# Performance work log

Hardware: AMD Instinct MI355X
Metric: run time of the kernel (lower is better)

The kernel has to match this reference:

```python
import jax, jax.numpy as jnp
import numpy as np

B, S, D_IN, D_OUT = 4, 8192, 1024, 1024


def setup_inputs() -> dict:
    key = jax.random.key(0)
    k1, k2, k3, k4 = jax.random.split(key, 4)
    x = jax.random.normal(k1, (B, S, D_IN), dtype=jnp.float32)
    # signed int8 weights, stored int8 as in the torch buffer
    weight_int = jax.random.randint(k2, (D_OUT, D_IN), -128, 128, dtype=jnp.int32).astype(jnp.int8)
    # realistic per-output-channel scales
    weight_scale = jax.random.uniform(k3, (D_OUT,), dtype=jnp.float32, minval=0.005, maxval=0.02)
    input_scale = jnp.asarray(0.05, dtype=jnp.float32)
    bias = jax.random.normal(k4, (D_OUT,), dtype=jnp.float32) * 0.01
    return {"x": x, "weight_int": weight_int, "weight_scale": weight_scale,
            "input_scale": input_scale, "bias": bias}


def reference(x, weight_int, weight_scale, input_scale, bias):
    # quantize activations to int8 (faithful: round, clamp, cast)
    x_int = jnp.clip(jnp.round(x / input_scale), -128, 127).astype(jnp.int8)
    # module upcasts both operands to fp32 for the matmul
    out = jnp.matmul(x_int.astype(jnp.float32), weight_int.astype(jnp.float32).T)
    # dequantize: per-output-channel weight scale * scalar input scale, then bias
    out = out * weight_scale * input_scale + bias
    return out
```

## Files before the change

### kernel.cpp

```cpp
#include <hip/hip_runtime.h>
#include <stdint.h>
#include <stddef.h>

typedef int   v4i __attribute__((ext_vector_type(4)));
typedef float v4f __attribute__((ext_vector_type(4)));

#define BM 128
#define BN 128
#define BKB 128
#define M_DIM 32768
#define N_DIM 1024
#define K_DIM 1024

typedef const __attribute__((address_space(1))) void gvoid_t;
typedef __attribute__((address_space(3))) void lvoid_t;

__device__ __forceinline__ void gload16(const void* g, void* l) {
    __builtin_amdgcn_global_load_lds((gvoid_t*)g, (lvoid_t*)l, 16, 0, 0);
}

__global__ __launch_bounds__(256)
void repack_w_kernel(const int* __restrict__ wi, int* __restrict__ wq, int n4)
{
    int i = blockIdx.x * blockDim.x + threadIdx.x;
    if (i < n4) {
        v4i v = ((const v4i*)wi)[i];
        wq[i] = (v[0] & 255) | ((v[1] & 255) << 8) |
                ((v[2] & 255) << 16) | ((v[3] & 255) << 24);
    }
}

__global__ __launch_bounds__(256, 2)
void quant_kernel(const float* __restrict__ x, int* __restrict__ q,
                  const float* __restrict__ iscale_p, int n4)
{
    const float is = *iscale_p;
    int idx = blockIdx.x * blockDim.x + threadIdx.x;
    int stride = gridDim.x * blockDim.x;
    const v4f* xp = (const v4f*)x;
    for (int i = idx; i < n4; i += stride) {
        v4f v = xp[i];
        int r = 0;
        #pragma unroll
        for (int j = 0; j < 4; ++j) {
            float t = rintf(v[j] / is);
            t = fminf(127.f, fmaxf(-128.f, t));
            r |= ((int)t & 255) << (8 * j);
        }
        q[i] = r;
    }
}

__global__ __launch_bounds__(256, 2)
void qgemm_kernel(const signed char* __restrict__ Aq,
                  const signed char* __restrict__ W,
                  const float* __restrict__ wscale,
                  const float* __restrict__ iscale_p,
                  const float* __restrict__ bias,
                  float* __restrict__ out)
{
    __shared__ signed char lA[BM * BKB];
    __shared__ signed char lB[BN * BKB];

    const int nwg = gridDim.x;
    const int bid = blockIdx.x;
    const int wg  = (bid & 7) * (nwg >> 3) + (bid >> 3);
    const int m_blk = wg >> 3;
    const int n_blk = wg & 7;
    const int mrow0 = m_blk * BM;
    const int ncol0 = n_blk * BN;

    const int tid = threadIdx.x;
    const int wv  = tid >> 6;
    const int ln  = tid & 63;
    const int wm  = wv >> 1;
    const int wn  = wv & 1;
    const int lrow = ln & 15;
    const int lk16 = (ln >> 4) << 4;
    const int swz  = (lrow & 7) << 4;

    v4i acc[4][4] = {};

    for (int kt = 0; kt < K_DIM; kt += BKB) {
        __syncthreads();
        #pragma unroll
        for (int c = 0; c < 4; ++c) {
            const int o   = c * 4096 + wv * 1024 + ln * 16;
            const int row = o >> 7;
            const int inr = (o & 127) ^ ((row & 7) << 4);
            gload16(Aq + (size_t)(mrow0 + row) * K_DIM + kt + inr,
                    (void*)(lA + c * 4096 + wv * 1024));
            gload16(W + (size_t)(ncol0 + row) * K_DIM + kt + inr,
                    (void*)(lB + c * 4096 + wv * 1024));
        }
        __syncthreads();
        #pragma unroll
        for (int st = 0; st < 2; ++st) {
            v4i af[4], bf[4];
            #pragma unroll
            for (int i = 0; i < 4; ++i) {
                const int arow = wm * 64 + i * 16 + lrow;
                af[i] = *(const v4i*)&lA[arow * BKB + ((st * 64 + lk16) ^ swz)];
                const int brow = wn * 64 + i * 16 + lrow;
                bf[i] = *(const v4i*)&lB[brow * BKB + ((st * 64 + lk16) ^ swz)];
            }
            #pragma unroll
            for (int i = 0; i < 4; ++i)
                #pragma unroll
                for (int j = 0; j < 4; ++j)
                    acc[i][j] = __builtin_amdgcn_mfma_i32_16x16x64_i8(
                                    af[i], bf[j], acc[i][j], 0, 0, 0);
        }
    }

    const float is = *iscale_p;
    const int r0 = mrow0 + wm * 64 + ((ln >> 4) << 2);
    const int c0 = ncol0 + wn * 64 + lrow;
    #pragma unroll
    for (int j = 0; j < 4; ++j) {
        const int col = c0 + j * 16;
        const float sc = wscale[col] * is;
        const float bv = bias[col];
        #pragma unroll
        for (int i = 0; i < 4; ++i) {
            const int row = r0 + i * 16;
            #pragma unroll
            for (int r = 0; r < 4; ++r)
                out[(size_t)(row + r) * N_DIM + col] = (float)acc[i][j][r] * sc + bv;
        }
    }
}

extern "C" void kernel_launch(void* const* d_in, const int* in_sizes, int n_in,
                              void* d_out, int out_size, void* d_ws, size_t ws_size,
                              hipStream_t stream)
{
    const float* x       = (const float*)d_in[0];
    const int*   w32     = (const int*)d_in[1];
    const float* wscale  = (const float*)d_in[2];
    const float* iscale  = (const float*)d_in[3];
    const float* bias    = (const float*)d_in[4];
    float* out           = (float*)d_out;

    signed char* aq = (signed char*)d_ws;
    signed char* wq = (signed char*)d_ws + (size_t)M_DIM * K_DIM;

    const int wn4 = (N_DIM * K_DIM) / 4;
    repack_w_kernel<<<(wn4 + 255) / 256, 256, 0, stream>>>(w32, (int*)wq, wn4);

    quant_kernel<<<8192, 256, 0, stream>>>(x, (int*)aq, iscale, (M_DIM * K_DIM) / 4);

    const int grid = (M_DIM / BM) * (N_DIM / BN);
    qgemm_kernel<<<grid, 256, 0, stream>>>(aq, wq, wscale, iscale, bias, out);
}
```

Before: 85.49 us.

## Fuse activation quantization into the int8 GEMM with a fragment-packed weight layout

Removes the standalone quantization kernel and its int8 activation buffer. Each 512-thread block now quantizes a 64-row slab of x straight into a swizzled 64KB LDS tile, then loops over all N tiles. Weights are repacked once into MFMA fragment order so each lane reads B fragments straight from global memory (L2) instead of staging them in LDS. This drops the intermediate activation write and read, but every block now streams the whole weight matrix from cache. It also uses a large LDS footprint and replaces the divide with multiplication by a reciprocal, which can change rounding at exact ties.

Result: faster. 77.94 us (-8.8%).

```diff
diff --git a/kernel.cpp b/kernel.cpp
--- a/kernel.cpp
+++ b/kernel.cpp
@@ -5,128 +5,108 @@
 typedef int   v4i __attribute__((ext_vector_type(4)));
 typedef float v4f __attribute__((ext_vector_type(4)));
 
-#define BM 128
-#define BN 128
-#define BKB 128
 #define M_DIM 32768
 #define N_DIM 1024
 #define K_DIM 1024
+#define BM 64
+#define NTILES 8
+#define KSTEPS 16
 
-typedef const __attribute__((address_space(1))) void gvoid_t;
-typedef __attribute__((address_space(3))) void lvoid_t;
-
-__device__ __forceinline__ void gload16(const void* g, void* l) {
-    __builtin_amdgcn_global_load_lds((gvoid_t*)g, (lvoid_t*)l, 16, 0, 0);
+__global__ __launch_bounds__(256)
+void repack_w_kernel(const int* __restrict__ w32, int* __restrict__ wf)
+{
+    const int i  = blockIdx.x * 256 + threadIdx.x;
+    const int f  = i >> 8;
+    const int r  = i & 255;
+    const int ln = r >> 2;
+    const int dw = r & 3;
+    const int jj = f & 1;
+    const int wn = (f >> 1) & 3;
+    const int ks = (f >> 3) & 15;
+    const int nt = f >> 7;
+    const int n  = nt * 128 + wn * 32 + jj * 16 + (ln & 15);
+    const int k  = ks * 64 + (ln >> 4) * 16 + dw * 4;
+    const v4i v  = *(const v4i*)&w32[(size_t)n * K_DIM + k];
+    wf[i] = (v[0] & 255) | ((v[1] & 255) << 8) |
+            ((v[2] & 255) << 16) | ((v[3] & 255) << 24);
 }
 
-__global__ __launch_bounds__(256)
-void repack_w_kernel(const int* __restrict__ wi, int* __restrict__ wq, int n4)
-{
-    int i = blockIdx.x * blockDim.x + threadIdx.x;
-    if (i < n4) {
-        v4i v = ((const v4i*)wi)[i];
-        wq[i] = (v[0] & 255) | ((v[1] & 255) << 8) |
-                ((v[2] & 255) << 16) | ((v[3] & 255) << 24);
-    }
-}
-
-__global__ __launch_bounds__(256, 2)
-void quant_kernel(const float* __restrict__ x, int* __restrict__ q,
-                  const float* __restrict__ iscale_p, int n4)
-{
-    const float is = *iscale_p;
-    int idx = blockIdx.x * blockDim.x + threadIdx.x;
-    int stride = gridDim.x * blockDim.x;
-    const v4f* xp = (const v4f*)x;
-    for (int i = idx; i < n4; i += stride) {
-        v4f v = xp[i];
-        int r = 0;
-        #pragma unroll
-        for (int j = 0; j < 4; ++j) {
-            float t = rintf(v[j] / is);
-            t = fminf(127.f, fmaxf(-128.f, t));
-            r |= ((int)t & 255) << (8 * j);
-        }
-        q[i] = r;
-    }
-}
-
-__global__ __launch_bounds__(256, 2)
-void qgemm_kernel(const signed char* __restrict__ Aq,
-                  const signed char* __restrict__ W,
+__global__ __launch_bounds__(512, 4)
+void fused_kernel(const float* __restrict__ x,
+                  const signed char* __restrict__ Wf,
                   const float* __restrict__ wscale,
                   const float* __restrict__ iscale_p,
                   const float* __restrict__ bias,
                   float* __restrict__ out)
 {
-    __shared__ signed char lA[BM * BKB];
-    __shared__ signed char lB[BN * BKB];
+    __shared__ signed char lA[BM * K_DIM];
 
-    const int nwg = gridDim.x;
-    const int bid = blockIdx.x;
-    const int wg  = (bid & 7) * (nwg >> 3) + (bid >> 3);
-    const int m_blk = wg >> 3;
-    const int n_blk = wg & 7;
-    const int mrow0 = m_blk * BM;
-    const int ncol0 = n_blk * BN;
+    const int mrow0 = blockIdx.x * BM;
+    const int t  = threadIdx.x;
+    const int wv = t >> 6;
+    const int ln = t & 63;
+    const int wm = wv >> 2;
+    const int wn = wv & 3;
 
-    const int tid = threadIdx.x;
-    const int wv  = tid >> 6;
-    const int ln  = tid & 63;
-    const int wm  = wv >> 1;
-    const int wn  = wv & 1;
-    const int lrow = ln & 15;
-    const int lk16 = (ln >> 4) << 4;
-    const int swz  = (lrow & 7) << 4;
+    {
+        const float inv = 1.0f / *iscale_p;
+        const int colf = (t & 255) * 4;
+        const int rsub = t >> 8;
+        for (int j = 0; j < 32; ++j) {
+            const int row = j * 2 + rsub;
+            const v4f v = *(const v4f*)&x[(size_t)(mrow0 + row) * K_DIM + colf];
+            int r = 0;
+            #pragma unroll
+            for (int e = 0; e < 4; ++e) {
+                float q = rintf(v[e] * inv);
+                q = fminf(127.f, fmaxf(-128.f, q));
+                r |= ((int)q & 255) << (8 * e);
+            }
+            *(int*)&lA[row * K_DIM + (colf ^ ((row & 7) << 4))] = r;
+        }
+    }
+    __syncthreads();
 
-    v4i acc[4][4] = {};
+    const int lr = ln & 15;
+    const int kh = (ln >> 4) * 16;
+    const float is = *iscale_p;
 
-    for (int kt = 0; kt < K_DIM; kt += BKB) {
-        __syncthreads();
-        #pragma unroll
-        for (int c = 0; c < 4; ++c) {
-            const int o   = c * 4096 + wv * 1024 + ln * 16;
-            const int row = o >> 7;
-            const int inr = (o & 127) ^ ((row & 7) << 4);
-            gload16(Aq + (size_t)(mrow0 + row) * K_DIM + kt + inr,
-                    (void*)(lA + c * 4096 + wv * 1024));
-            gload16(W + (size_t)(ncol0 + row) * K_DIM + kt + inr,
-                    (void*)(lB + c * 4096 + wv * 1024));
-        }
-        __syncthreads();
-        #pragma unroll
-        for (int st = 0; st < 2; ++st) {
-            v4i af[4], bf[4];
+    for (int nt = 0; nt < NTILES; ++nt) {
+        v4i acc[2][2] = {};
+        #pragma unroll 4
+        for (int ks = 0; ks < KSTEPS; ++ks) {
+            v4i aF[2], bF[2];
             #pragma unroll
-            for (int i = 0; i < 4; ++i) {
-                const int arow = wm * 64 + i * 16 + lrow;
-                af[i] = *(const v4i*)&lA[arow * BKB + ((st * 64 + lk16) ^ swz)];
-                const int brow = wn * 64 + i * 16 + lrow;
-                bf[i] = *(const v4i*)&lB[brow * BKB + ((st * 64 + lk16) ^ swz)];
+            for (int i = 0; i < 2; ++i) {
+                const int row = wm * 32 + i * 16 + lr;
+                aF[i] = *(const v4i*)&lA[row * K_DIM +
+                                         ((ks * 64 + kh) ^ ((row & 7) << 4))];
             }
             #pragma unroll
-            for (int i = 0; i < 4; ++i)
+            for (int j = 0; j < 2; ++j) {
+                const int f = (nt * 16 + ks) * 8 + wn * 2 + j;
+                bF[j] = *(const v4i*)&Wf[(size_t)f * 1024 + ln * 16];
+            }
+            #pragma unroll
+            for (int i = 0; i < 2; ++i)
                 #pragma unroll
-                for (int j = 0; j < 4; ++j)
+                for (int j = 0; j < 2; ++j)
                     acc[i][j] = __builtin_amdgcn_mfma_i32_16x16x64_i8(
-                                    af[i], bf[j], acc[i][j], 0, 0, 0);
+                                    aF[i], bF[j], acc[i][j], 0, 0, 0);
         }
-    }
-
-    const float is = *iscale_p;
-    const int r0 = mrow0 + wm * 64 + ((ln >> 4) << 2);
-    const int c0 = ncol0 + wn * 64 + lrow;
-    #pragma unroll
-    for (int j = 0; j < 4; ++j) {
-        const int col = c0 + j * 16;
-        const float sc = wscale[col] * is;
-        const float bv = bias[col];
         #pragma unroll
-        for (int i = 0; i < 4; ++i) {
-            const int row = r0 + i * 16;
+        for (int j = 0; j < 2; ++j) {
+            const int col = nt * 128 + wn * 32 + j * 16 + lr;
+            const float sc = wscale[col] * is;
+            const float bv = bias[col];
             #pragma unroll
-            for (int r = 0; r < 4; ++r)
-                out[(size_t)(row + r) * N_DIM + col] = (float)acc[i][j][r] * sc + bv;
+            for (int i = 0; i < 2; ++i) {
+                const int rowb = mrow0 + wm * 32 + i * 16 + ((ln >> 4) << 2);
+                #pragma unroll
+                for (int r = 0; r < 4; ++r)
+                    out[(size_t)(rowb + r) * N_DIM + col] =
+                        (float)acc[i][j][r] * sc + bv;
+            }
         }
     }
 }
@@ -142,14 +122,9 @@
     const float* bias    = (const float*)d_in[4];
     float* out           = (float*)d_out;
 
-    signed char* aq = (signed char*)d_ws;
-    signed char* wq = (signed char*)d_ws + (size_t)M_DIM * K_DIM;
+    signed char* wf = (signed char*)d_ws;
 
-    const int wn4 = (N_DIM * K_DIM) / 4;
-    repack_w_kernel<<<(wn4 + 255) / 256, 256, 0, stream>>>(w32, (int*)wq, wn4);
+    repack_w_kernel<<<(N_DIM * K_DIM / 4) / 256, 256, 0, stream>>>(w32, (int*)wf);
 
-    quant_kernel<<<8192, 256, 0, stream>>>(x, (int*)aq, iscale, (M_DIM * K_DIM) / 4);
-
-    const int grid = (M_DIM / BM) * (N_DIM / BN);
-    qgemm_kernel<<<grid, 256, 0, stream>>>(aq, wq, wscale, iscale, bias, out);
+    fused_kernel<<<M_DIM / BM, 512, 0, stream>>>(x, wf, wscale, iscale, bias, out);
 }
```
